# Optimization experiments

Hardware: AMD Instinct MI355X
Metric: run time of the kernel (lower is better)

## Reference

```python
import jax, jax.numpy as jnp
import numpy as np

B, S, D = 2, 2048, 2048
N_HEADS, N_KV_HEADS, HEAD_DIM = 16, 8, 128
N_REP = N_HEADS // N_KV_HEADS
EPS = 1e-6
SCALE = HEAD_DIM ** -0.5


def setup_inputs() -> dict:
    key = jax.random.key(0)
    ks = jax.random.split(key, 6)
    x = jax.random.normal(ks[0], (B, S, D), dtype=jnp.float32)
    # RoPE frequencies (Llama-style cis stored as interleaved [cos, sin])
    inv_freq = 1.0 / (1e6 ** (jnp.arange(0, HEAD_DIM, 2, dtype=jnp.float32) / HEAD_DIM))
    angles = jnp.arange(S, dtype=jnp.float32)[:, None] * inv_freq[None, :]  # [S, HEAD_DIM//2]
    freqs_cis = jnp.stack([jnp.cos(angles), jnp.sin(angles)], axis=-1)  # [S, HEAD_DIM//2, 2]
    wq = jax.random.normal(ks[1], (N_HEADS * HEAD_DIM, D), dtype=jnp.float32) * 0.02
    wk = jax.random.normal(ks[2], (N_KV_HEADS * HEAD_DIM, D), dtype=jnp.float32) * 0.02
    wv = jax.random.normal(ks[3], (N_KV_HEADS * HEAD_DIM, D), dtype=jnp.float32) * 0.02
    wo = jax.random.normal(ks[4], (D, N_HEADS * HEAD_DIM), dtype=jnp.float32) * 0.02
    q_norm_w = jnp.ones((HEAD_DIM,), dtype=jnp.float32)
    k_norm_w = jnp.ones((HEAD_DIM,), dtype=jnp.float32)
    return {"x": x, "freqs_cis": freqs_cis, "wq": wq, "wk": wk, "wv": wv,
            "wo": wo, "q_norm_w": q_norm_w, "k_norm_w": k_norm_w}


def _rmsnorm(t, w):
    var = jnp.mean(jnp.square(t), axis=-1, keepdims=True)
    return t * jax.lax.rsqrt(var + EPS) * w


def _apply_rope(t, cos, sin):
    # t: [B, S, H, HEAD_DIM]; cos/sin: [1, S, 1, HEAD_DIM//2]
    tp = t.reshape(*t.shape[:-1], HEAD_DIM // 2, 2)
    tr, ti = tp[..., 0], tp[..., 1]
    out = jnp.stack([tr * cos - ti * sin, tr * sin + ti * cos], axis=-1)
    return out.reshape(t.shape)


def reference(x, freqs_cis, wq, wk, wv, wo, q_norm_w, k_norm_w):
    bs, seqlen, _ = x.shape
    xq = (x @ wq.T).reshape(bs, seqlen, N_HEADS, HEAD_DIM)
    xk = (x @ wk.T).reshape(bs, seqlen, N_KV_HEADS, HEAD_DIM)
    xv = (x @ wv.T).reshape(bs, seqlen, N_KV_HEADS, HEAD_DIM)
    # per-head RMSNorm (Qwen3)
    xq = _rmsnorm(xq, q_norm_w)
    xk = _rmsnorm(xk, k_norm_w)
    # rotary embedding
    cos = freqs_cis[:seqlen, :, 0][None, :, None, :]
    sin = freqs_cis[:seqlen, :, 1][None, :, None, :]
    xq = _apply_rope(xq, cos, sin)
    xk = _apply_rope(xk, cos, sin)
    # GQA: repeat kv heads
    keys = jnp.repeat(xk, N_REP, axis=2)    # [B, S, N_HEADS, HEAD_DIM]
    values = jnp.repeat(xv, N_REP, axis=2)
    q = xq.transpose(0, 2, 1, 3)   # [B, H, S, D]
    k = keys.transpose(0, 2, 1, 3)
    v = values.transpose(0, 2, 1, 3)
    scores = jnp.einsum("bhqd,bhkd->bhqk", q, k) * SCALE
    causal = jnp.tril(jnp.ones((seqlen, seqlen), dtype=bool))
    scores = jnp.where(causal[None, None], scores, jnp.finfo(scores.dtype).min)
    attn = jax.nn.softmax(scores, axis=-1)
    out = jnp.einsum("bhqk,bhkd->bhqd", attn, v)
    out = out.transpose(0, 2, 1, 3).reshape(bs, seqlen, N_HEADS * HEAD_DIM)
    return out @ wo.T
```

## Files before the change

kernel.cpp:

```cpp
#include <hip/hip_runtime.h>

#define B_ 2
#define S_ 2048
#define D_ 2048
#define NH 16
#define NKV 8
#define HD 128
#define SCALE 0.08838834764831845f
#define CEXP 0.1275255f
#define RTHR 62.733f

typedef unsigned short u16;
typedef __attribute__((ext_vector_type(8))) short short8;
typedef __attribute__((ext_vector_type(4))) float f32x4;
typedef __attribute__((ext_vector_type(16))) float f32x16;
typedef __attribute__((ext_vector_type(4))) int i32x4;
typedef __attribute__((ext_vector_type(2))) int i32x2;

#define ASM_VMCNT(N) asm volatile("s_waitcnt vmcnt(" #N ")" ::: "memory")

__device__ __forceinline__ u16 f2b(float f) {
  union { float f; unsigned u; } c; c.f = f;
  unsigned u = c.u;
  return (u16)((u + 0x7fffu + ((u >> 16) & 1u)) >> 16);
}
__device__ __forceinline__ float b2f(u16 h) {
  union { unsigned u; float f; } c; c.u = ((unsigned)h) << 16;
  return c.f;
}
__device__ __forceinline__ float exp2f_fast(float x) {
  float r; asm("v_exp_f32 %0, %1" : "=v"(r) : "v"(x)); return r;
}
__device__ __forceinline__ int cvtpk(float a, float b) {
  int r; asm("v_cvt_pk_bf16_f32 %0, %1, %2" : "=v"(r) : "v"(a), "v"(b)); return r;
}
__device__ __forceinline__ void pl32swap(int& a, int& b) {
  asm volatile("v_permlane32_swap_b32 %0, %1" : "+v"(a), "+v"(b));
}

__device__ __forceinline__ void load_lds16(const u16* g, u16* l) {
  __builtin_amdgcn_global_load_lds(
      (const __attribute__((address_space(1))) unsigned int*)g,
      (__attribute__((address_space(3))) unsigned int*)l, 16, 0, 0);
}

__global__ __launch_bounds__(256) void cvt_all(const float* __restrict__ x,
                                               const float* __restrict__ wq,
                                               const float* __restrict__ wk,
                                               const float* __restrict__ wv,
                                               const float* __restrict__ wo,
                                               u16* __restrict__ xb,
                                               u16* __restrict__ wqkvb,
                                               u16* __restrict__ wob) {
  const int blk = blockIdx.x;
  const float* src; u16* dst; int base;
  if (blk < 8192)       { src = x;  dst = xb;                  base = blk; }
  else if (blk < 12288) { src = wq; dst = wqkvb;               base = blk - 8192; }
  else if (blk < 14336) { src = wk; dst = wqkvb + 2048 * 2048; base = blk - 12288; }
  else if (blk < 16384) { src = wv; dst = wqkvb + 3072 * 2048; base = blk - 14336; }
  else                  { src = wo; dst = wob;                 base = blk - 16384; }
  int i = base * 256 + threadIdx.x;
  float4 v = ((const float4*)src)[i];
  u16 o0 = f2b(v.x), o1 = f2b(v.y), o2 = f2b(v.z), o3 = f2b(v.w);
  unsigned long long packed = (unsigned long long)o0 | ((unsigned long long)o1 << 16) |
                              ((unsigned long long)o2 << 32) | ((unsigned long long)o3 << 48);
  ((unsigned long long*)dst)[i] = packed;
}

template<int OUTF32>
__global__ __launch_bounds__(256, 2) void gemm_bt2(const u16* __restrict__ A, const u16* __restrict__ Bm,
                                                   void* __restrict__ Cv, int M, int N, int K, int nbn) {
  __shared__ __align__(16) u16 As[2][128 * 64];
  __shared__ __align__(16) u16 Bs[2][128 * 64];
  const int tid = threadIdx.x;
  const int wave = tid >> 6, lane = tid & 63;
  const int nwg = gridDim.x, cpx = nwg >> 3;
  const int L = (blockIdx.x & 7) * cpx + (blockIdx.x >> 3);
  const int bm = L / nbn, bn = L % nbn;
  const int wr = wave >> 1, wc = wave & 1;
  const int r = lane & 15, hi = lane >> 4;

  f32x4 acc[4][4];
#pragma unroll
  for (int m = 0; m < 4; ++m)
#pragma unroll
    for (int n = 0; n < 4; ++n) acc[m][n] = (f32x4){0.f, 0.f, 0.f, 0.f};

  const int gslot = (lane & 7) ^ (lane >> 3);
  const int srow = lane >> 3;

  auto stage = [&](int buf, int k0) {
#pragma unroll
    for (int jj = 0; jj < 4; ++jj) {
      int j = wave * 4 + jj;
      int row = j * 8 + srow;
      load_lds16(A + (size_t)(bm * 128 + row) * K + k0 + gslot * 8, &As[buf][j * 512]);
      load_lds16(Bm + (size_t)(bn * 128 + row) * K + k0 + gslot * 8, &Bs[buf][j * 512]);
    }
  };

  const int nk = K >> 6;
  stage(0, 0);
  for (int kt = 0; kt < nk; ++kt) {
    if (kt + 1 < nk) {
      stage((kt + 1) & 1, (kt + 1) << 6);
      ASM_VMCNT(8);
    } else {
      ASM_VMCNT(0);
    }
    __builtin_amdgcn_sched_barrier(0);
    __builtin_amdgcn_s_barrier();
    __builtin_amdgcn_sched_barrier(0);
    const u16* as = As[kt & 1];
    const u16* bs = Bs[kt & 1];
#pragma unroll
    for (int kc = 0; kc < 2; ++kc) {
      short8 af[4], bfr[4];
#pragma unroll
      for (int m = 0; m < 4; ++m) {
        int row = wr * 64 + m * 16 + r;
        int slot = (hi + kc * 4) ^ (row & 7);
        af[m] = *(const short8*)&as[row * 64 + slot * 8];
      }
#pragma unroll
      for (int n = 0; n < 4; ++n) {
        int row = wc * 64 + n * 16 + r;
        int slot = (hi + kc * 4) ^ (row & 7);
        bfr[n] = *(const short8*)&bs[row * 64 + slot * 8];
      }
#pragma unroll
      for (int m = 0; m < 4; ++m)
#pragma unroll
        for (int n = 0; n < 4; ++n)
          acc[m][n] = __builtin_amdgcn_mfma_f32_16x16x32_bf16(af[m], bfr[n], acc[m][n], 0, 0, 0);
    }
    __builtin_amdgcn_sched_barrier(0);
    __builtin_amdgcn_s_barrier();
    __builtin_amdgcn_sched_barrier(0);
  }

#pragma unroll
  for (int m = 0; m < 4; ++m)
#pragma unroll
    for (int n = 0; n < 4; ++n)
#pragma unroll
      for (int r2 = 0; r2 < 4; ++r2) {
        int grow = bm * 128 + wr * 64 + m * 16 + hi * 4 + r2;
        int gcol = bn * 128 + wc * 64 + n * 16 + r;
        if (OUTF32)
          ((float*)Cv)[(size_t)grow * N + gcol] = acc[m][n][r2];
        else
          ((u16*)Cv)[(size_t)grow * N + gcol] = f2b(acc[m][n][r2]);
      }
}

__global__ __launch_bounds__(256) void rmsnorm_rope(const u16* __restrict__ qkv, const float* __restrict__ fc,
                                                    const float* __restrict__ qw, const float* __restrict__ kw,
                                                    u16* __restrict__ qr, u16* __restrict__ kr) {
  const int tid = threadIdx.x, wave = tid >> 6, lane = tid & 63;
  const int rowid = blockIdx.x * 4 + wave;
  const int token = rowid / 24;
  const int hh = rowid % 24;
  const int b = token >> 11, s = token & 2047;
  const bool isq = hh < 16;
  const int off = isq ? hh * 128 : 2048 + (hh - 16) * 128;
  const u16* src = qkv + (size_t)token * 4096 + off + lane * 2;
  unsigned pv = *(const unsigned*)src;
  float t0 = b2f((u16)(pv & 0xffffu));
  float t1 = b2f((u16)(pv >> 16));
  float ss = t0 * t0 + t1 * t1;
#pragma unroll
  for (int mm = 1; mm < 64; mm <<= 1) ss += __shfl_xor(ss, mm, 64);
  float rms = rsqrtf(ss * (1.0f / 128.0f) + 1e-6f);
  const float* nw = isq ? qw : kw;
  t0 *= rms * nw[lane * 2];
  t1 *= rms * nw[lane * 2 + 1];
  float c = fc[(s * 64 + lane) * 2], sn = fc[(s * 64 + lane) * 2 + 1];
  float o0 = t0 * c - t1 * sn;
  float o1 = t0 * sn + t1 * c;
  unsigned ov = (unsigned)f2b(o0) | ((unsigned)f2b(o1) << 16);
  if (isq)
    *(unsigned*)(qr + ((size_t)(b * 16 + hh) * 2048 + s) * 128 + lane * 2) = ov;
  else
    *(unsigned*)(kr + ((size_t)(b * 8 + hh - 16) * 2048 + s) * 128 + lane * 2) = ov;
}

__global__ __launch_bounds__(256) void v_transpose(const u16* __restrict__ qkv, u16* __restrict__ vt,
                                                   int* __restrict__ ctr) {
  if (blockIdx.x == 0 && threadIdx.x == 0) *ctr = 0;
  __shared__ __align__(16) u16 tile[64][136];
  const int blk = blockIdx.x;
  const int st = blk & 31, h = (blk >> 5) & 7, b = blk >> 8;
  const int s0 = st * 64, t = threadIdx.x;
#pragma unroll
  for (int p = 0; p < 4; ++p) {
    int row = p * 16 + (t >> 4), c8 = (t & 15) * 8;
    const u16* src = qkv + (size_t)(b * 2048 + s0 + row) * 4096 + 3072 + h * 128 + c8;
    *(short8*)&tile[row][c8] = *(const short8*)src;
  }
  __syncthreads();
  const int d = t >> 1, j0 = (t & 1) * 32;
  u16* dst = vt + ((size_t)(b * 8 + h) * 128 + d) * 2048 + s0 + j0;
#pragma unroll
  for (int j = 0; j < 32; j += 8) {
    short8 v;
#pragma unroll
    for (int u = 0; u < 8; ++u) v[u] = (short)tile[j0 + j + u][d];
    *(short8*)(dst + j) = v;
  }
}

__global__ __launch_bounds__(256, 2) void attn4(const u16* __restrict__ qr, const u16* __restrict__ kr,
                                                const u16* __restrict__ vt, u16* __restrict__ ao,
                                                int* __restrict__ ctr) {
  __shared__ __align__(16) u16 Ks[2][64 * 128];
  __shared__ __align__(16) u16 Vs[2][128 * 64];
  __shared__ int tileno;
  const int tid = threadIdx.x, wave = tid >> 6, lane = tid & 63;
  const int ql = lane & 31, lh = lane >> 5;

  for (;;) {
    if (tid == 0) tileno = atomicAdd(ctr, 1);
    __syncthreads();
    const int n = tileno;
    if (n >= 512) break;
    const int t = 15 - (n >> 5);
    const int bh = n & 31;
    const int b = bh >> 4, h = bh & 15, hkv = h >> 1;

    const u16* Q  = qr + (size_t)(b * 16 + h) * S_ * HD;
    const u16* Kg = kr + (size_t)(b * 8 + hkv) * S_ * HD;
    const u16* Vg = vt + (size_t)(b * 8 + hkv) * HD * S_;

    const int q0w = t * 128 + wave * 32;
    const int nsteps = 2 * (t + 1);

    short8 qf[8];
#pragma unroll
    for (int ki = 0; ki < 8; ++ki)
      qf[ki] = *(const short8*)(Q + (size_t)(q0w + ql) * HD + ki * 16 + lh * 8);

    f32x16 o[4];
#pragma unroll
    for (int dt = 0; dt < 4; ++dt) o[dt] = 0.f;
    float m = -1e30f, l = 0.f;

    auto stage = [&](int buf, int kv0) {
#pragma unroll
      for (int inst = 0; inst < 4; ++inst) {
        int p = wave * 4096 + inst * 1024 + lane * 16;
        int row = p >> 8;
        int colb = (p & 255) ^ ((row & 7) << 4);
        load_lds16(Kg + (((size_t)(kv0 + row)) << 7) + (colb >> 1),
                   &Ks[buf][(wave * 4096 + inst * 1024) >> 1]);
      }
#pragma unroll
      for (int inst = 0; inst < 4; ++inst) {
        int p = wave * 4096 + inst * 1024 + lane * 16;
        int d = p >> 7;
        int colb = (p & 127) ^ ((d & 7) << 4);
        load_lds16(Vg + (size_t)d * S_ + kv0 + (colb >> 1),
                   &Vs[buf][(wave * 4096 + inst * 1024) >> 1]);
      }
    };

    stage(0, 0);
    for (int i = 0; i < nsteps; ++i) {
      const int kv0 = i * 64;
      const u16* kb = Ks[i & 1];
      const u16* vb = Vs[i & 1];
      if (i + 1 < nsteps) {
        stage((i + 1) & 1, kv0 + 64);
        ASM_VMCNT(8);
      } else {
        ASM_VMCNT(0);
      }
      __builtin_amdgcn_sched_barrier(0);
      __builtin_amdgcn_s_barrier();
      __builtin_amdgcn_sched_barrier(0);

      if (kv0 < q0w + 32) {
        f32x16 sacc[2];
        sacc[0] = 0.f; sacc[1] = 0.f;
        __builtin_amdgcn_s_setprio(1);
#pragma unroll
        for (int ki = 0; ki < 8; ++ki) {
          const int off = ki * 32 + lh * 16;
#pragma unroll
          for (int kvt = 0; kvt < 2; ++kvt) {
            const int row = kvt * 32 + ql;
            short8 kf = *(const short8*)&kb[(row << 7) + ((off ^ ((row & 7) << 4)) >> 1)];
            sacc[kvt] = __builtin_amdgcn_mfma_f32_32x32x16_bf16(kf, qf[ki], sacc[kvt], 0, 0, 0);
          }
        }
        __builtin_amdgcn_s_setprio(0);
        const int q = q0w + ql;
        if (kv0 + 64 > q0w) {
#pragma unroll
          for (int kvt = 0; kvt < 2; ++kvt) {
            const int kvb = kv0 + kvt * 32 + 4 * lh;
#pragma unroll
            for (int reg = 0; reg < 16; ++reg) {
              const int kvr = kvb + (reg & 3) + 8 * (reg >> 2);
              sacc[kvt][reg] = (kvr > q) ? -1e30f : sacc[kvt][reg];
            }
          }
        }
        float mx = sacc[0][0];
#pragma unroll
        for (int kvt = 0; kvt < 2; ++kvt)
#pragma unroll
          for (int reg = 0; reg < 16; ++reg) mx = fmaxf(mx, sacc[kvt][reg]);
        mx = fmaxf(mx, __shfl_xor(mx, 32, 64));
        if (__any(mx > m + RTHR)) {
          float mn = fmaxf(m, mx);
          float sc = exp2f_fast((m - mn) * CEXP);
          l *= sc;
          m = mn;
#pragma unroll
          for (int dt = 0; dt < 4; ++dt)
#pragma unroll
            for (int reg = 0; reg < 16; ++reg) o[dt][reg] *= sc;
        }
        short8 pf[4];
        const float mc = m * CEXP;
        float ps = 0.f;
#pragma unroll
        for (int kvt = 0; kvt < 2; ++kvt) {
          float p[16];
#pragma unroll
          for (int reg = 0; reg < 16; ++reg) {
            p[reg] = exp2f_fast(__builtin_fmaf(sacc[kvt][reg], CEXP, -mc));
            ps += p[reg];
          }
          int A0 = cvtpk(p[0], p[1]),  B0 = cvtpk(p[2], p[3]);
          int C0 = cvtpk(p[4], p[5]),  D0 = cvtpk(p[6], p[7]);
          int A1 = cvtpk(p[8], p[9]),  B1 = cvtpk(p[10], p[11]);
          int C1 = cvtpk(p[12], p[13]), D1 = cvtpk(p[14], p[15]);
          pl32swap(A0, C0);
          pl32swap(B0, D0);
          pl32swap(A1, C1);
          pl32swap(B1, D1);
          i32x4 w0 = (i32x4){A0, B0, C0, D0};
          i32x4 w1 = (i32x4){A1, B1, C1, D1};
          pf[kvt * 2]     = *(short8*)&w0;
          pf[kvt * 2 + 1] = *(short8*)&w1;
        }
        l += ps;
        __builtin_amdgcn_s_setprio(1);
#pragma unroll
        for (int kc = 0; kc < 4; ++kc) {
          const int off = kc * 32 + lh * 16;
#pragma unroll
          for (int dt = 0; dt < 4; ++dt) {
            const int d = dt * 32 + ql;
            short8 vf = *(const short8*)&vb[(d << 6) + ((off ^ ((d & 7) << 4)) >> 1)];
            o[dt] = __builtin_amdgcn_mfma_f32_32x32x16_bf16(vf, pf[kc], o[dt], 0, 0, 0);
          }
        }
        __builtin_amdgcn_s_setprio(0);
      }
      __builtin_amdgcn_sched_barrier(0);
      __builtin_amdgcn_s_barrier();
      __builtin_amdgcn_sched_barrier(0);
    }

    l += __shfl_xor(l, 32, 64);
    const float inv = 1.0f / l;
    const size_t rowoff = ((size_t)(b * 2048 + q0w + ql)) * 2048 + h * 128;
#pragma unroll
    for (int dt = 0; dt < 4; ++dt)
#pragma unroll
      for (int g = 0; g < 4; ++g) {
        const int d0 = dt * 32 + 8 * g + 4 * lh;
        int w0 = cvtpk(o[dt][4 * g] * inv, o[dt][4 * g + 1] * inv);
        int w1 = cvtpk(o[dt][4 * g + 2] * inv, o[dt][4 * g + 3] * inv);
        i32x2 pk = (i32x2){w0, w1};
        *(i32x2*)((u16*)ao + rowoff + d0) = pk;
      }
    __syncthreads();
  }
}

extern "C" void kernel_launch(void* const* d_in, const int* in_sizes, int n_in,
                              void* d_out, int out_size, void* d_ws, size_t ws_size,
                              hipStream_t stream) {
  const float* x = (const float*)d_in[0];
  const float* fc = (const float*)d_in[1];
  const float* wq = (const float*)d_in[2];
  const float* wk = (const float*)d_in[3];
  const float* wv = (const float*)d_in[4];
  const float* wo = (const float*)d_in[5];
  const float* qw = (const float*)d_in[6];
  const float* kw = (const float*)d_in[7];
  float* out = (float*)d_out;
  char* ws = (char*)d_ws;

  u16* xb    = (u16*)(ws);
  u16* wqkvb = (u16*)(ws + 16777216);
  u16* wob   = (u16*)(ws + 33554432);
  u16* qkv   = (u16*)(ws + 41943040);
  u16* qrope = (u16*)(ws + 75497472);
  u16* krope = (u16*)(ws + 92274688);
  u16* vtb   = (u16*)(ws + 100663296);
  u16* ao    = (u16*)(ws + 109051904);
  int* ctr   = (int*)qkv;

  cvt_all<<<20480, 256, 0, stream>>>(x, wq, wk, wv, wo, xb, wqkvb, wob);

  gemm_bt2<0><<<1024, 256, 0, stream>>>(xb, wqkvb, (void*)qkv, 4096, 4096, 2048, 32);

  rmsnorm_rope<<<24576, 256, 0, stream>>>(qkv, fc, qw, kw, qrope, krope);
  v_transpose<<<512, 256, 0, stream>>>(qkv, vtb, ctr);

  attn4<<<448, 256, 0, stream>>>(qrope, krope, vtb, ao, ctr);

  gemm_bt2<1><<<512, 256, 0, stream>>>(ao, wob, (void*)out, 4096, 2048, 2048, 16);
}
```

Measured before the change: 227.5 us.

## Replace atomic work queue with static paired causal tiles and XCD-aware mapping

The attention kernel no longer pulls tiles from a global atomic counter. Each of 256 blocks handles a fixed pair of query tiles (t and 15-t), which balances causal work per block. The block-to-(batch, head) mapping groups heads by XCD so K/V stay local in each XCD's L2. This removes the atomic, the shared broadcast and a per-tile barrier, but the static schedule cannot absorb runtime imbalance, and 256 blocks may underfill the GPU compared with the previous 448-block persistent launch.

```diff
diff --git a/kernel.cpp b/kernel.cpp
--- a/kernel.cpp
+++ b/kernel.cpp
@@ -185,9 +185,7 @@
     *(unsigned*)(kr + ((size_t)(b * 8 + hh - 16) * 2048 + s) * 128 + lane * 2) = ov;
 }
 
-__global__ __launch_bounds__(256) void v_transpose(const u16* __restrict__ qkv, u16* __restrict__ vt,
-                                                   int* __restrict__ ctr) {
-  if (blockIdx.x == 0 && threadIdx.x == 0) *ctr = 0;
+__global__ __launch_bounds__(256) void v_transpose(const u16* __restrict__ qkv, u16* __restrict__ vt) {
   __shared__ __align__(16) u16 tile[64][136];
   const int blk = blockIdx.x;
   const int st = blk & 31, h = (blk >> 5) & 7, b = blk >> 8;
@@ -210,28 +208,44 @@
   }
 }
 
-__global__ __launch_bounds__(256, 2) void attn4(const u16* __restrict__ qr, const u16* __restrict__ kr,
-                                                const u16* __restrict__ vt, u16* __restrict__ ao,
-                                                int* __restrict__ ctr) {
+__global__ __launch_bounds__(256, 2) void attn5(const u16* __restrict__ qr, const u16* __restrict__ kr,
+                                                const u16* __restrict__ vt, u16* __restrict__ ao) {
   __shared__ __align__(16) u16 Ks[2][64 * 128];
   __shared__ __align__(16) u16 Vs[2][128 * 64];
-  __shared__ int tileno;
   const int tid = threadIdx.x, wave = tid >> 6, lane = tid & 63;
   const int ql = lane & 31, lh = lane >> 5;
 
-  for (;;) {
-    if (tid == 0) tileno = atomicAdd(ctr, 1);
-    __syncthreads();
-    const int n = tileno;
-    if (n >= 512) break;
-    const int t = 15 - (n >> 5);
-    const int bh = n & 31;
-    const int b = bh >> 4, h = bh & 15, hkv = h >> 1;
-
-    const u16* Q  = qr + (size_t)(b * 16 + h) * S_ * HD;
-    const u16* Kg = kr + (size_t)(b * 8 + hkv) * S_ * HD;
-    const u16* Vg = vt + (size_t)(b * 8 + hkv) * HD * S_;
-
+  const int xcd = blockIdx.x & 7, idx = blockIdx.x >> 3;
+  const int bh = xcd * 4 + (idx & 3);
+  const int p = idx >> 2;
+  const int b = bh >> 4, h = bh & 15, hkv = h >> 1;
+
+  const u16* Q  = qr + (size_t)(b * 16 + h) * S_ * HD;
+  const u16* Kg = kr + (size_t)(b * 8 + hkv) * S_ * HD;
+  const u16* Vg = vt + (size_t)(b * 8 + hkv) * HD * S_;
+
+  auto stage = [&](int buf, int kv0) {
+#pragma unroll
+    for (int inst = 0; inst < 4; ++inst) {
+      int pp = wave * 4096 + inst * 1024 + lane * 16;
+      int row = pp >> 8;
+      int colb = (pp & 255) ^ ((row & 7) << 4);
+      load_lds16(Kg + (((size_t)(kv0 + row)) << 7) + (colb >> 1),
+                 &Ks[buf][(wave * 4096 + inst * 1024) >> 1]);
+    }
+#pragma unroll
+    for (int inst = 0; inst < 4; ++inst) {
+      int pp = wave * 4096 + inst * 1024 + lane * 16;
+      int d = pp >> 7;
+      int colb = (pp & 127) ^ ((d & 7) << 4);
+      load_lds16(Vg + (size_t)d * S_ + kv0 + (colb >> 1),
+                 &Vs[buf][(wave * 4096 + inst * 1024) >> 1]);
+    }
+  };
+
+#pragma unroll 1
+  for (int half = 0; half < 2; ++half) {
+    const int t = half ? p : 15 - p;
     const int q0w = t * 128 + wave * 32;
     const int nsteps = 2 * (t + 1);
 
@@ -244,25 +258,6 @@
 #pragma unroll
     for (int dt = 0; dt < 4; ++dt) o[dt] = 0.f;
     float m = -1e30f, l = 0.f;
-
-    auto stage = [&](int buf, int kv0) {
-#pragma unroll
-      for (int inst = 0; inst < 4; ++inst) {
-        int p = wave * 4096 + inst * 1024 + lane * 16;
-        int row = p >> 8;
-        int colb = (p & 255) ^ ((row & 7) << 4);
-        load_lds16(Kg + (((size_t)(kv0 + row)) << 7) + (colb >> 1),
-                   &Ks[buf][(wave * 4096 + inst * 1024) >> 1]);
-      }
-#pragma unroll
-      for (int inst = 0; inst < 4; ++inst) {
-        int p = wave * 4096 + inst * 1024 + lane * 16;
-        int d = p >> 7;
-        int colb = (p & 127) ^ ((d & 7) << 4);
-        load_lds16(Vg + (size_t)d * S_ + kv0 + (colb >> 1),
-                   &Vs[buf][(wave * 4096 + inst * 1024) >> 1]);
-      }
-    };
 
     stage(0, 0);
     for (int i = 0; i < nsteps; ++i) {
@@ -327,16 +322,16 @@
         float ps = 0.f;
 #pragma unroll
         for (int kvt = 0; kvt < 2; ++kvt) {
-          float p[16];
+          float pv[16];
 #pragma unroll
           for (int reg = 0; reg < 16; ++reg) {
-            p[reg] = exp2f_fast(__builtin_fmaf(sacc[kvt][reg], CEXP, -mc));
-            ps += p[reg];
+            pv[reg] = exp2f_fast(__builtin_fmaf(sacc[kvt][reg], CEXP, -mc));
+            ps += pv[reg];
           }
-          int A0 = cvtpk(p[0], p[1]),  B0 = cvtpk(p[2], p[3]);
-          int C0 = cvtpk(p[4], p[5]),  D0 = cvtpk(p[6], p[7]);
-          int A1 = cvtpk(p[8], p[9]),  B1 = cvtpk(p[10], p[11]);
-          int C1 = cvtpk(p[12], p[13]), D1 = cvtpk(p[14], p[15]);
+          int A0 = cvtpk(pv[0], pv[1]),  B0 = cvtpk(pv[2], pv[3]);
+          int C0 = cvtpk(pv[4], pv[5]),  D0 = cvtpk(pv[6], pv[7]);
+          int A1 = cvtpk(pv[8], pv[9]),  B1 = cvtpk(pv[10], pv[11]);
+          int C1 = cvtpk(pv[12], pv[13]), D1 = cvtpk(pv[14], pv[15]);
           pl32swap(A0, C0);
           pl32swap(B0, D0);
           pl32swap(A1, C1);
@@ -378,7 +373,6 @@
         i32x2 pk = (i32x2){w0, w1};
         *(i32x2*)((u16*)ao + rowoff + d0) = pk;
       }
-    __syncthreads();
   }
 }
 
@@ -404,16 +398,15 @@
   u16* krope = (u16*)(ws + 92274688);
   u16* vtb   = (u16*)(ws + 100663296);
   u16* ao    = (u16*)(ws + 109051904);
-  int* ctr   = (int*)qkv;
 
   cvt_all<<<20480, 256, 0, stream>>>(x, wq, wk, wv, wo, xb, wqkvb, wob);
 
   gemm_bt2<0><<<1024, 256, 0, stream>>>(xb, wqkvb, (void*)qkv, 4096, 4096, 2048, 32);
 
   rmsnorm_rope<<<24576, 256, 0, stream>>>(qkv, fc, qw, kw, qrope, krope);
-  v_transpose<<<512, 256, 0, stream>>>(qkv, vtb, ctr);
-
-  attn4<<<448, 256, 0, stream>>>(qrope, krope, vtb, ao, ctr);
+  v_transpose<<<512, 256, 0, stream>>>(qkv, vtb);
+
+  attn5<<<256, 256, 0, stream>>>(qrope, krope, vtb, ao);
 
   gemm_bt2<1><<<512, 256, 0, stream>>>(ao, wob, (void*)out, 4096, 2048, 2048, 16);
 }
```

Result: no change. 224.9 us (-1.2%).
